# Optimization experiments

Measured on AMD Instinct MI355X. Metric: run time of the kernel, lower is better.

## Reference

```python
import jax, jax.numpy as jnp
import numpy as np

N_NODES = 100000
N_EDGES = 1600000


def setup_inputs() -> dict:
    key = jax.random.key(0)
    ks = jax.random.split(key, 6)
    x = jax.random.normal(ks[0], (N_NODES, 166), dtype=jnp.float32)
    edge_index = jax.random.randint(ks[1], (2, N_EDGES), 0, N_NODES, dtype=jnp.int64)
    s = 0.05
    return {
        "x": x,
        "edge_index": edge_index,
        "W1l": jax.random.normal(ks[2], (166, 128), dtype=jnp.float32) * s,
        "b1": jnp.zeros((128,), dtype=jnp.float32),
        "W1r": jax.random.normal(ks[3], (166, 128), dtype=jnp.float32) * s,
        "W2l": jax.random.normal(ks[4], (128, 2), dtype=jnp.float32) * s,
        "b2": jnp.zeros((2,), dtype=jnp.float32),
        "W2r": jax.random.normal(ks[5], (128, 2), dtype=jnp.float32) * s,
    }


def _sage_mean_agg(h, src, dst, n_nodes):
    # mean over incoming edges (PyG SAGEConv default aggr='mean');
    # nodes with no in-edges get zeros.
    summed = jax.ops.segment_sum(h[src], dst, num_segments=n_nodes)
    deg = jax.ops.segment_sum(jnp.ones_like(dst, dtype=h.dtype), dst,
                              num_segments=n_nodes)
    return summed / jnp.maximum(deg, 1.0)[:, None]


def reference(x, edge_index, W1l, b1, W1r, W2l, b2, W2r):
    src, dst = edge_index[0], edge_index[1]
    n = x.shape[0]
    # layer 1: out = lin_l(mean_agg(x)) + lin_r(x)
    agg1 = _sage_mean_agg(x, src, dst, n)
    h = agg1 @ W1l + b1 + x @ W1r
    h = jax.nn.relu(h)
    # dropout p=0.5 is identity in eval mode
    # layer 2
    agg2 = _sage_mean_agg(h, src, dst, n)
    out = agg2 @ W2l + b2 + h @ W2r
    return jax.nn.log_softmax(out, axis=1)
```

## Files before the change

### kernel.cpp

```cpp
#include <hip/hip_runtime.h>
#include <hip/hip_bf16.h>
#include <math.h>

#define N_NODES 100000
#define N_EDGES 1600000
#define FDIM 166
#define HDIM 128
#define KP 192
#define CAP 48
#define MBLK 64
#define NXCD 8
#define NODES_PER (N_NODES / NXCD)

typedef __attribute__((ext_vector_type(8))) short bf16x8;
typedef __attribute__((ext_vector_type(4))) float f32x4;

__device__ inline float bf2f(unsigned short s) {
    unsigned int u = ((unsigned int)s) << 16;
    float f; __builtin_memcpy(&f, &u, 4); return f;
}
__device__ inline float bflo(unsigned int u) {
    unsigned int v = u << 16;
    float f; __builtin_memcpy(&f, &v, 4); return f;
}
__device__ inline float bfhi(unsigned int u) {
    unsigned int v = u & 0xffff0000u;
    float f; __builtin_memcpy(&f, &v, 4); return f;
}
__device__ inline unsigned short f2bf(float f) {
    unsigned int u; __builtin_memcpy(&u, &f, 4);
    unsigned int r = u + 0x7fffu + ((u >> 16) & 1u);
    return (unsigned short)(r >> 16);
}
__device__ inline bf16x8 pack8(float4 a, float4 b) {
    union { bf16x8 v; __hip_bfloat162 h[4]; } u;
    u.h[0] = __float22bfloat162_rn(make_float2(a.x, a.y));
    u.h[1] = __float22bfloat162_rn(make_float2(a.z, a.w));
    u.h[2] = __float22bfloat162_rn(make_float2(b.x, b.y));
    u.h[3] = __float22bfloat162_rn(make_float2(b.z, b.w));
    return u.v;
}

__global__ void k_pre(const float* __restrict__ W1l, const float* __restrict__ W1r,
                      unsigned short* __restrict__ wt2, int* __restrict__ cnt) {
    int idx = blockIdx.x * 256 + threadIdx.x;
    if (blockIdx.x < 192) {
        int fb = idx >> 9, r = idx & 511;
        int lane = r >> 3, j = r & 7;
        int g = lane >> 4, l15 = lane & 15;
        int kk = fb / 16, cb = fb & 15;
        int c = cb * 16 + l15;
        int k = kk * 32 + 8 * g + j;
        float v = 0.f;
        if (k < FDIM)
            v = (c < HDIM) ? W1l[k * HDIM + c] : W1r[k * HDIM + (c - HDIM)];
        wt2[idx] = f2bf(v);
    } else {
        int i = idx - 192 * 256;
        if (i < N_NODES) cnt[i] = 0;
    }
}

__global__ __launch_bounds__(256) void k_fill(const int* __restrict__ ei,
                                              int* __restrict__ cnt,
                                              int* __restrict__ adj) {
    int xcd = blockIdx.x & (NXCD - 1);
    int grp = blockIdx.x >> 3;
    int lo = xcd * NODES_PER, hi = lo + NODES_PER;
    int stride = (gridDim.x >> 3) * 256;
    for (int e = grp * 256 + threadIdx.x; e < N_EDGES; e += stride) {
        int d = ei[N_EDGES + e];
        int s = ei[e];
        if (d >= lo && d < hi) {
            int slot = atomicAdd(&cnt[d], 1);
            if (slot < CAP) adj[d * CAP + slot] = s;
        }
    }
}

__global__ __launch_bounds__(256, 3) void k_gemm(
        const float* __restrict__ x, const unsigned short* __restrict__ wt2,
        unsigned short* __restrict__ yl, unsigned short* __restrict__ yr) {
    int tid = threadIdx.x;
    int r0 = blockIdx.x * MBLK;
    int w = tid >> 6, lane = tid & 63;

    int rbase = (w >> 1) * 32;
    int half = w & 1;
    int l15 = lane & 15, g = lane >> 4;

    int gr0 = r0 + rbase + l15;       if (gr0 > N_NODES - 1) gr0 = N_NODES - 1;
    int gr1 = gr0 + 16;               if (gr1 > N_NODES - 1) gr1 = N_NODES - 1;
    const char* xr0 = (const char*)x + (size_t)gr0 * (FDIM * 4) + 32 * g;
    const char* xr1 = (const char*)x + (size_t)gr1 * (FDIM * 4) + 32 * g;

    f32x4 acc[2][8];
    #pragma unroll
    for (int a = 0; a < 2; a++)
        #pragma unroll
        for (int b = 0; b < 8; b++) acc[a][b] = (f32x4){0.f, 0.f, 0.f, 0.f};

    const char* wb = (const char*)wt2 + (size_t)lane * 16;

    for (int kk = 0; kk < 6; ++kk) {
        bf16x8 ww[8];
        #pragma unroll
        for (int cf = 0; cf < 8; cf++)
            ww[cf] = *(const bf16x8*)(wb + (size_t)(kk * 16 + half * 8 + cf) * 1024);
        float4 p0, q0, p1, q1;
        if (kk < 5) {
            p0 = *(const float4*)(xr0 + kk * 128);
            q0 = *(const float4*)(xr0 + kk * 128 + 16);
            p1 = *(const float4*)(xr1 + kk * 128);
            q1 = *(const float4*)(xr1 + kk * 128 + 16);
        } else {
            if (g == 0) {
                p0 = *(const float4*)(xr0 + 640);
                p1 = *(const float4*)(xr1 + 640);
                float2 t0 = *(const float2*)(xr0 + 656);
                float2 t1 = *(const float2*)(xr1 + 656);
                q0 = make_float4(t0.x, t0.y, 0.f, 0.f);
                q1 = make_float4(t1.x, t1.y, 0.f, 0.f);
            } else {
                p0 = make_float4(0.f, 0.f, 0.f, 0.f);
                q0 = p0; p1 = p0; q1 = p0;
            }
        }
        bf16x8 xb0 = pack8(p0, q0);
        bf16x8 xb1 = pack8(p1, q1);
        #pragma unroll
        for (int cf = 0; cf < 8; cf++) {
            acc[0][cf] = __builtin_amdgcn_mfma_f32_16x16x32_bf16(ww[cf], xb0, acc[0][cf], 0, 0, 0);
            acc[1][cf] = __builtin_amdgcn_mfma_f32_16x16x32_bf16(ww[cf], xb1, acc[1][cf], 0, 0, 0);
        }
    }

    unsigned short* dst = half ? yr : yl;
    #pragma unroll
    for (int rf = 0; rf < 2; rf++) {
        int gr = r0 + rbase + 16 * rf + l15;
        if (gr < N_NODES) {
            #pragma unroll
            for (int cf = 0; cf < 8; cf++) {
                ushort4 o;
                o.x = f2bf(acc[rf][cf][0]); o.y = f2bf(acc[rf][cf][1]);
                o.z = f2bf(acc[rf][cf][2]); o.w = f2bf(acc[rf][cf][3]);
                *(ushort4*)&dst[(size_t)gr * HDIM + 16 * cf + 4 * g] = o;
            }
        }
    }
}

__global__ __launch_bounds__(256) void k_agg1(
        const unsigned short* __restrict__ yl, const unsigned short* __restrict__ yr,
        const int* __restrict__ cnt, const int* __restrict__ adj,
        const float* __restrict__ b1,
        const float* __restrict__ W2l, const float* __restrict__ W2r,
        float* __restrict__ zw) {
    int w = threadIdx.x >> 6, lane = threadIdx.x & 63;
    int i = blockIdx.x * 4 + w;
    if (i >= N_NODES) return;
    int deg = cnt[i];
    int n = min(deg, CAP);
    int aidx = adj[i * CAP + lane];
    float a0 = 0.f, a1 = 0.f, p0 = 0.f, p1 = 0.f, q0 = 0.f, q1 = 0.f, r0 = 0.f, r1 = 0.f;
    int j = 0;
    for (; j + 4 <= n; j += 4) {
        int s0 = __shfl(aidx, j, 64);
        int s1 = __shfl(aidx, j + 1, 64);
        int s2 = __shfl(aidx, j + 2, 64);
        int s3 = __shfl(aidx, j + 3, 64);
        unsigned int u0 = *(const unsigned int*)&yl[(size_t)s0 * HDIM + lane * 2];
        unsigned int u1 = *(const unsigned int*)&yl[(size_t)s1 * HDIM + lane * 2];
        unsigned int u2 = *(const unsigned int*)&yl[(size_t)s2 * HDIM + lane * 2];
        unsigned int u3 = *(const unsigned int*)&yl[(size_t)s3 * HDIM + lane * 2];
        a0 += bflo(u0); a1 += bfhi(u0);
        p0 += bflo(u1); p1 += bfhi(u1);
        q0 += bflo(u2); q1 += bfhi(u2);
        r0 += bflo(u3); r1 += bfhi(u3);
    }
    for (; j < n; ++j) {
        int s = __shfl(aidx, j, 64);
        unsigned int u = *(const unsigned int*)&yl[(size_t)s * HDIM + lane * 2];
        a0 += bflo(u); a1 += bfhi(u);
    }
    a0 += p0 + q0 + r0;
    a1 += p1 + q1 + r1;
    float inv = 1.f / (float)max(deg, 1);
    unsigned int ur = *(const unsigned int*)&yr[(size_t)i * HDIM + lane * 2];
    float2 bb = *(const float2*)&b1[lane * 2];
    float h0 = fmaxf(a0 * inv + bflo(ur) + bb.x, 0.f);
    float h1 = fmaxf(a1 * inv + bfhi(ur) + bb.y, 0.f);
    float4 wl2 = *(const float4*)&W2l[lane * 4];
    float4 wr2 = *(const float4*)&W2r[lane * 4];
    float z0 = h0 * wl2.x + h1 * wl2.z;
    float z1 = h0 * wl2.y + h1 * wl2.w;
    float w0 = h0 * wr2.x + h1 * wr2.z;
    float w1 = h0 * wr2.y + h1 * wr2.w;
    #pragma unroll
    for (int m = 32; m; m >>= 1) {
        z0 += __shfl_xor(z0, m, 64); z1 += __shfl_xor(z1, m, 64);
        w0 += __shfl_xor(w0, m, 64); w1 += __shfl_xor(w1, m, 64);
    }
    if (lane == 0) {
        float4 o = {z0, z1, w0, w1};
        *(float4*)&zw[i * 4] = o;
    }
}

__global__ void k_out(const float* __restrict__ zw, const int* __restrict__ cnt,
                      const int* __restrict__ adj, const float* __restrict__ b2,
                      float* __restrict__ out) {
    int i = blockIdx.x * 256 + threadIdx.x;
    if (i >= N_NODES) return;
    int deg = cnt[i];
    int n = min(deg, CAP);
    float s0 = 0.f, s1 = 0.f;
    const int* arow = adj + i * CAP;
    for (int j = 0; j < n; j++) {
        int s = arow[j];
        float2 zz = *(const float2*)&zw[s * 4];
        s0 += zz.x; s1 += zz.y;
    }
    float inv = 1.f / (float)max(deg, 1);
    float p0 = s0 * inv + b2[0] + zw[i * 4 + 2];
    float p1 = s1 * inv + b2[1] + zw[i * 4 + 3];
    float mx = fmaxf(p0, p1);
    float lse = mx + logf(expf(p0 - mx) + expf(p1 - mx));
    out[i * 2 + 0] = p0 - lse;
    out[i * 2 + 1] = p1 - lse;
}

extern "C" void kernel_launch(void* const* d_in, const int* in_sizes, int n_in,
                              void* d_out, int out_size, void* d_ws, size_t ws_size,
                              hipStream_t stream) {
    const float* x   = (const float*)d_in[0];
    const int*   ei  = (const int*)d_in[1];
    const float* W1l = (const float*)d_in[2];
    const float* b1  = (const float*)d_in[3];
    const float* W1r = (const float*)d_in[4];
    const float* W2l = (const float*)d_in[5];
    const float* b2  = (const float*)d_in[6];
    const float* W2r = (const float*)d_in[7];
    float* out = (float*)d_out;

    char* ws = (char*)d_ws;
    size_t off = 0;
    auto alloc = [&](size_t bytes) {
        off = (off + 255) & ~(size_t)255;
        void* p = ws + off;
        off += bytes;
        return p;
    };
    int* cnt            = (int*)alloc((size_t)N_NODES * 4);
    int* adj            = (int*)alloc((size_t)N_NODES * CAP * 4);
    unsigned short* wt2 = (unsigned short*)alloc((size_t)256 * KP * 2);
    unsigned short* yl  = (unsigned short*)alloc((size_t)N_NODES * HDIM * 2);
    unsigned short* yr  = (unsigned short*)alloc((size_t)N_NODES * HDIM * 2);
    float* zw           = (float*)alloc((size_t)N_NODES * 4 * 4);
    (void)ws_size; (void)in_sizes; (void)n_in; (void)out_size;

    k_pre<<<192 + (N_NODES + 255) / 256, 256, 0, stream>>>(W1l, W1r, wt2, cnt);
    k_fill<<<2048, 256, 0, stream>>>(ei, cnt, adj);
    k_gemm<<<(N_NODES + MBLK - 1) / MBLK, 256, 0, stream>>>(x, wt2, yl, yr);
    k_agg1<<<(N_NODES + 3) / 4, 256, 0, stream>>>(yl, yr, cnt, adj, b1, W2l, W2r, zw);
    k_out<<<(N_NODES + 255) / 256, 256, 0, stream>>>(zw, cnt, adj, b2, out);
}
```

Measured before the change: 202.0 us.

## Unroll edge-fill loop, fully unroll GEMM k-loop, split z/w arrays

The adjacency-fill kernel now loads four edges per iteration before issuing atomics, so more loads are in flight and latency is hidden better. The GEMM k-loop is fully unrolled. The layer-2 projections are split into separate z and w arrays, so the neighbour gather in k_out touches a denser 8-byte-per-node array instead of a 16-byte stride. The risks are higher register pressure in the unrolled GEMM, which could cut occupancy, and little gain from the small kernels.

```diff
diff --git a/kernel.cpp b/kernel.cpp
--- a/kernel.cpp
+++ b/kernel.cpp
@@ -68,12 +68,32 @@
     int grp = blockIdx.x >> 3;
     int lo = xcd * NODES_PER, hi = lo + NODES_PER;
     int stride = (gridDim.x >> 3) * 256;
-    for (int e = grp * 256 + threadIdx.x; e < N_EDGES; e += stride) {
-        int d = ei[N_EDGES + e];
-        int s = ei[e];
-        if (d >= lo && d < hi) {
-            int slot = atomicAdd(&cnt[d], 1);
-            if (slot < CAP) adj[d * CAP + slot] = s;
+    int e0 = grp * 256 + threadIdx.x;
+    for (int e = e0; e < N_EDGES; e += 4 * stride) {
+        int eB = e + stride, eC = e + 2 * stride, eD = e + 3 * stride;
+        int dA = ei[N_EDGES + e];
+        int dB = (eB < N_EDGES) ? ei[N_EDGES + eB] : -1;
+        int dC = (eC < N_EDGES) ? ei[N_EDGES + eC] : -1;
+        int dD = (eD < N_EDGES) ? ei[N_EDGES + eD] : -1;
+        int sA = ei[e];
+        int sB = (eB < N_EDGES) ? ei[eB] : 0;
+        int sC = (eC < N_EDGES) ? ei[eC] : 0;
+        int sD = (eD < N_EDGES) ? ei[eD] : 0;
+        if (dA >= lo && dA < hi) {
+            int slot = atomicAdd(&cnt[dA], 1);
+            if (slot < CAP) adj[dA * CAP + slot] = sA;
+        }
+        if (dB >= lo && dB < hi) {
+            int slot = atomicAdd(&cnt[dB], 1);
+            if (slot < CAP) adj[dB * CAP + slot] = sB;
+        }
+        if (dC >= lo && dC < hi) {
+            int slot = atomicAdd(&cnt[dC], 1);
+            if (slot < CAP) adj[dC * CAP + slot] = sC;
+        }
+        if (dD >= lo && dD < hi) {
+            int slot = atomicAdd(&cnt[dD], 1);
+            if (slot < CAP) adj[dD * CAP + slot] = sD;
         }
     }
 }
@@ -102,6 +122,7 @@
 
     const char* wb = (const char*)wt2 + (size_t)lane * 16;
 
+    #pragma unroll
     for (int kk = 0; kk < 6; ++kk) {
         bf16x8 ww[8];
         #pragma unroll
@@ -156,7 +177,7 @@
         const int* __restrict__ cnt, const int* __restrict__ adj,
         const float* __restrict__ b1,
         const float* __restrict__ W2l, const float* __restrict__ W2r,
-        float* __restrict__ zw) {
+        float* __restrict__ zarr, float* __restrict__ warr) {
     int w = threadIdx.x >> 6, lane = threadIdx.x & 63;
     int i = blockIdx.x * 4 + w;
     if (i >= N_NODES) return;
@@ -203,14 +224,14 @@
         w0 += __shfl_xor(w0, m, 64); w1 += __shfl_xor(w1, m, 64);
     }
     if (lane == 0) {
-        float4 o = {z0, z1, w0, w1};
-        *(float4*)&zw[i * 4] = o;
-    }
-}
-
-__global__ void k_out(const float* __restrict__ zw, const int* __restrict__ cnt,
-                      const int* __restrict__ adj, const float* __restrict__ b2,
-                      float* __restrict__ out) {
+        *(float2*)&zarr[i * 2] = make_float2(z0, z1);
+        *(float2*)&warr[i * 2] = make_float2(w0, w1);
+    }
+}
+
+__global__ void k_out(const float* __restrict__ zarr, const float* __restrict__ warr,
+                      const int* __restrict__ cnt, const int* __restrict__ adj,
+                      const float* __restrict__ b2, float* __restrict__ out) {
     int i = blockIdx.x * 256 + threadIdx.x;
     if (i >= N_NODES) return;
     int deg = cnt[i];
@@ -219,12 +240,12 @@
     const int* arow = adj + i * CAP;
     for (int j = 0; j < n; j++) {
         int s = arow[j];
-        float2 zz = *(const float2*)&zw[s * 4];
+        float2 zz = *(const float2*)&zarr[s * 2];
         s0 += zz.x; s1 += zz.y;
     }
     float inv = 1.f / (float)max(deg, 1);
-    float p0 = s0 * inv + b2[0] + zw[i * 4 + 2];
-    float p1 = s1 * inv + b2[1] + zw[i * 4 + 3];
+    float p0 = s0 * inv + b2[0] + warr[i * 2 + 0];
+    float p1 = s1 * inv + b2[1] + warr[i * 2 + 1];
     float mx = fmaxf(p0, p1);
     float lse = mx + logf(expf(p0 - mx) + expf(p1 - mx));
     out[i * 2 + 0] = p0 - lse;
@@ -257,12 +278,13 @@
     unsigned short* wt2 = (unsigned short*)alloc((size_t)256 * KP * 2);
     unsigned short* yl  = (unsigned short*)alloc((size_t)N_NODES * HDIM * 2);
     unsigned short* yr  = (unsigned short*)alloc((size_t)N_NODES * HDIM * 2);
-    float* zw           = (float*)alloc((size_t)N_NODES * 4 * 4);
+    float* zarr         = (float*)alloc((size_t)N_NODES * 2 * 4);
+    float* warr         = (float*)alloc((size_t)N_NODES * 2 * 4);
     (void)ws_size; (void)in_sizes; (void)n_in; (void)out_size;
 
     k_pre<<<192 + (N_NODES + 255) / 256, 256, 0, stream>>>(W1l, W1r, wt2, cnt);
     k_fill<<<2048, 256, 0, stream>>>(ei, cnt, adj);
     k_gemm<<<(N_NODES + MBLK - 1) / MBLK, 256, 0, stream>>>(x, wt2, yl, yr);
-    k_agg1<<<(N_NODES + 3) / 4, 256, 0, stream>>>(yl, yr, cnt, adj, b1, W2l, W2r, zw);
-    k_out<<<(N_NODES + 255) / 256, 256, 0, stream>>>(zw, cnt, adj, b2, out);
-}
+    k_agg1<<<(N_NODES + 3) / 4, 256, 0, stream>>>(yl, yr, cnt, adj, b1, W2l, W2r, zarr, warr);
+    k_out<<<(N_NODES + 255) / 256, 256, 0, stream>>>(zarr, warr, cnt, adj, b2, out);
+}
```

New measurement: 203.4 us. Within noise of the previous version (+0.7%).
